# Optimization experiments

Hardware: AMD Instinct MI355X
Metric: run time of the kernel (lower is better)

## Reference

```python
import jax, jax.numpy as jnp
import numpy as np
from jax import lax

B, N = 2, 8192
H = W = 256
KNN_K = 33          # includes self, as in _computeDensity
RADIUS = 0.1
CUTOFF = 1.0        # cutOffThreshold: a dx^2 + b dy^2 + c dx dy <= cutoffC
WIN = 9             # fixed splat footprint (ellipse extents ~1-3 px, clamped at 15 in source)
EPS = 1e-8


def setup_inputs() -> dict:
    key = jax.random.key(0)
    k1, k2, k3, k4, k5 = jax.random.split(key, 5)
    points = jax.random.normal(k1, (B, N, 3), jnp.float32)
    # projected pixel coordinates, kept a few px inside the image
    proj_xy = jax.random.uniform(k2, (B, N, 2), jnp.float32, 4.0, W - 4.0)
    # ellipse coefficients a, b, c with 4ab - c^2 > 0 (valid ellipse)
    ab = jax.random.uniform(k3, (B, N, 2), jnp.float32, 0.1, 0.5)
    c = jax.random.uniform(k4, (B, N, 1), jnp.float32, -0.05, 0.05)
    ellipse_params = jnp.concatenate([ab, c], axis=-1)
    colors = jax.random.uniform(k5, (B, N, 3), jnp.float32)
    return {"points": points, "proj_xy": proj_xy,
            "ellipse_params": ellipse_params, "colors": colors}


def _compute_density(points):
    # faithful jax version of _computeDensity: KNN gaussian density
    r2 = RADIUS * RADIUS
    sq = jnp.sum(points * points, axis=-1)                      # [B,N]
    # pairwise squared distances [B,N,N]
    d2 = sq[:, :, None] + sq[:, None, :] - 2.0 * jnp.einsum('bnd,bmd->bnm', points, points)
    neg_d2k, _ = lax.top_k(-d2, KNN_K)                          # k nearest (incl. self)
    d2k = jnp.maximum(-neg_d2k[:, :, 1:], 0.0)                  # drop self, [B,N,K-1]
    w = jnp.exp(-d2k / r2 / 4.0)
    w = jnp.where(d2k > r2, 0.0, w)
    return jnp.sum(w, axis=-1)                                  # [B,N]


def reference(points, proj_xy, ellipse_params, colors):
    density = _compute_density(points)                          # [B,N]
    a = ellipse_params[..., 0]
    b = ellipse_params[..., 1]
    c = ellipse_params[..., 2]
    x = proj_xy[..., 0]
    y = proj_xy[..., 1]
    # _findEllipseBoundingBox extents, clamped at 15 as in the grad path
    den = 4.0 * a * b - c * c
    xE = jnp.minimum(jnp.sqrt(4.0 * b * CUTOFF / den), 15.0)    # [B,N]
    yE = jnp.minimum(jnp.sqrt(4.0 * a * CUTOFF / den), 15.0)

    # fixed WINxWIN footprint around floor(proj) (jit-friendly bbox)
    R = WIN // 2
    offs = jnp.arange(-R, R + 1, dtype=jnp.float32)
    ox, oy = jnp.meshgrid(offs, offs, indexing='ij')
    ox = ox.reshape(-1)                                         # [P]
    oy = oy.reshape(-1)
    x0 = jnp.floor(x)
    y0 = jnp.floor(y)
    px = x0[..., None] + ox                                     # [B,N,P]
    py = y0[..., None] + oy
    dx = px - x[..., None]
    dy = py - y[..., None]
    # elliptical gaussian splat weight, truncated at cutoff
    Q = a[..., None] * dx * dx + b[..., None] * dy * dy + c[..., None] * dx * dy
    inb = (px >= 0) & (px < W) & (py >= 0) & (py < H)
    bbox = (jnp.abs(dx) <= xE[..., None] + 1.0) & (jnp.abs(dy) <= yE[..., None] + 1.0)
    mask = inb & bbox & (Q <= CUTOFF)
    w = jnp.where(mask, jnp.exp(-0.5 * Q) * density[..., None], 0.0)  # [B,N,P]

    # scatter-accumulate weighted colors and weights per pixel
    pxi = jnp.clip(px.astype(jnp.int32), 0, W - 1)
    pyi = jnp.clip(py.astype(jnp.int32), 0, H - 1)
    bi = jnp.arange(B, dtype=jnp.int32)[:, None, None]
    flat = ((bi * H + pyi) * W + pxi).reshape(-1)               # [B*N*P]
    wc = (w[..., None] * colors[:, :, None, :]).reshape(-1, 3)
    wf = w.reshape(-1)
    img_c = jnp.zeros((B * H * W, 3), jnp.float32).at[flat].add(wc)
    img_w = jnp.zeros((B * H * W,), jnp.float32).at[flat].add(wf)
    image = img_c / (img_w[:, None] + EPS)
    return image.reshape(B, H, W, 3)
```

## Files before the change

### kernel.cpp

```cpp
#include <hip/hip_runtime.h>

#define NB  2
#define NP  8192
#define IMH 256
#define IMW 256
#define NBKT 1024

constexpr float R2F = 0.01f;
constexpr float BK_SCALE = 64.f;
constexpr float BK_OFF   = 8.f;
#define BK_PAD 7

__device__ __forceinline__ int bucket_of(float x) {
    int b = (int)floorf((x + BK_OFF) * BK_SCALE);
    return min(max(b, 0), NBKT - 1);
}

__global__ __launch_bounds__(256) void init_kernel(
    float4* __restrict__ out4, float4* __restrict__ imgw4)
{
    const int t = blockIdx.x * 256 + threadIdx.x;
    const float4 z4 = make_float4(0.f, 0.f, 0.f, 0.f);
    if (t < 98304) out4[t] = z4;
    if (t < 32768) imgw4[t] = z4;
}

__global__ __launch_bounds__(1024) void binsort_kernel(
    const float* __restrict__ pts, float4* __restrict__ sorted,
    int* __restrict__ sidx, int* __restrict__ offsets)
{
    __shared__ int cntA[NBKT], cntB[NBKT], cur[NBKT];
    const int b   = blockIdx.x;
    const int tid = threadIdx.x;
    const float* __restrict__ base = pts + (size_t)b * NP * 3;

    cntA[tid] = 0;
    __syncthreads();

    float xs[8], ys[8], zs[8]; int bks[8];
    #pragma unroll
    for (int k = 0; k < 8; ++k) {
        const int i = k * 1024 + tid;
        xs[k] = base[i * 3 + 0];
        ys[k] = base[i * 3 + 1];
        zs[k] = base[i * 3 + 2];
        bks[k] = bucket_of(xs[k]);
        atomicAdd(&cntA[bks[k]], 1);
    }
    __syncthreads();

    int* src = cntA; int* dst = cntB;
    for (int off = 1; off < NBKT; off <<= 1) {
        int v = src[tid];
        if (tid >= off) v += src[tid - off];
        dst[tid] = v;
        __syncthreads();
        int* tmp = src; src = dst; dst = tmp;
    }
    const int start = (tid == 0) ? 0 : src[tid - 1];
    offsets[b * (NBKT + 1) + tid] = start;
    if (tid == 0) offsets[b * (NBKT + 1) + NBKT] = NP;
    cur[tid] = start;
    __syncthreads();

    #pragma unroll
    for (int k = 0; k < 8; ++k) {
        const int i = k * 1024 + tid;
        const int slot = atomicAdd(&cur[bks[k]], 1);
        const float sq = __fadd_rn(__fadd_rn(__fmul_rn(xs[k], xs[k]),
                                             __fmul_rn(ys[k], ys[k])),
                                   __fmul_rn(zs[k], zs[k]));
        sorted[(size_t)b * NP + slot] = make_float4(xs[k], ys[k], zs[k], sq);
        sidx  [(size_t)b * NP + slot] = i;
    }
}

__global__ __launch_bounds__(256) void densplat_kernel(
    const float4* __restrict__ sorted, const int* __restrict__ sidx,
    const int* __restrict__ offsets,
    const float* __restrict__ proj, const float* __restrict__ ell,
    const float* __restrict__ cols,
    float* __restrict__ img_c, float* __restrict__ img_w)
{
    const int wave = threadIdx.x >> 6, lane = threadIdx.x & 63;
    const int w  = blockIdx.x * 4 + wave;
    const int s0 = w * 8;
    const int b  = s0 >> 13;
    const int sb = s0 & (NP - 1);
    const float4* __restrict__ sp = sorted + (size_t)b * NP;

    float xi[8], yi[8], zi[8], sqi[8], sum[8];
    #pragma unroll
    for (int t = 0; t < 8; ++t) {
        const float4 p = sp[sb + t];
        xi[t] = p.x; yi[t] = p.y; zi[t] = p.z; sqi[t] = p.w;
        sum[t] = 0.f;
    }
    const int blo = max(bucket_of(xi[0]) - BK_PAD, 0);
    const int bhi = min(bucket_of(xi[7]) + BK_PAD + 1, NBKT);
    const int jlo = offsets[b * (NBKT + 1) + blo];
    const int jhi = offsets[b * (NBKT + 1) + bhi];

    for (int jj = jlo + lane; jj < jhi; jj += 64) {
        const float4 pj = sp[jj];
        #pragma unroll
        for (int t = 0; t < 8; ++t) {
            const float dot = __fmaf_rn(zi[t], pj.z,
                              __fmaf_rn(yi[t], pj.y,
                              __fmul_rn(xi[t], pj.x)));
            const float d2 = __fsub_rn(__fadd_rn(sqi[t], pj.w),
                                       __fadd_rn(dot, dot));
            const float d2c = fmaxf(d2, 0.f);
            if (jj != sb + t && d2c <= R2F)
                sum[t] += expf(__fmul_rn(__fdiv_rn(d2c, R2F), -0.25f));
        }
    }

    #pragma unroll
    for (int t = 0; t < 8; ++t) {
        float s = sum[t];
        #pragma unroll
        for (int off2 = 32; off2; off2 >>= 1) s += __shfl_down(s, off2, 64);
        const float dens = __shfl(s, 0, 64);
        if (dens == 0.f) continue;

        const size_t gp = (size_t)b * NP + sidx[(size_t)b * NP + sb + t];
        const float x = proj[gp * 2 + 0], y = proj[gp * 2 + 1];
        const float a  = ell[gp * 3 + 0], bb = ell[gp * 3 + 1], c = ell[gp * 3 + 2];
        const float cr = cols[gp * 3 + 0], cg = cols[gp * 3 + 1], cb = cols[gp * 3 + 2];

        const float den = __fsub_rn(__fmul_rn(__fmul_rn(4.f, a), bb),
                                    __fmul_rn(c, c));
        const float xE = fminf(__fsqrt_rn(__fdiv_rn(__fmul_rn(4.f, bb), den)), 15.f);
        const float yE = fminf(__fsqrt_rn(__fdiv_rn(__fmul_rn(4.f, a),  den)), 15.f);
        const float xEp1 = __fadd_rn(xE, 1.f);
        const float yEp1 = __fadd_rn(yE, 1.f);
        const float x0 = floorf(x), y0 = floorf(y);

        for (int idx = lane; idx < 81; idx += 64) {
            const float ox = (float)(idx / 9) - 4.f;
            const float oy = (float)(idx % 9) - 4.f;
            const float px = __fadd_rn(x0, ox);
            const float py = __fadd_rn(y0, oy);
            if (px < 0.f || px >= 256.f || py < 0.f || py >= 256.f) continue;
            const float dx = __fsub_rn(px, x);
            const float dy = __fsub_rn(py, y);
            if (fabsf(dx) > xEp1 || fabsf(dy) > yEp1) continue;
            const float Q = __fadd_rn(__fadd_rn(__fmul_rn(__fmul_rn(a, dx), dx),
                                                __fmul_rn(__fmul_rn(bb, dy), dy)),
                                      __fmul_rn(__fmul_rn(c, dx), dy));
            if (!(Q <= 1.0f)) continue;
            const float wgt = __fmul_rn(expf(__fmul_rn(-0.5f, Q)), dens);
            const int pxi = (int)px, pyi = (int)py;
            const int flat = ((b << 8) + pyi) * IMW + pxi;
            atomicAdd(&img_c[flat * 3 + 0], __fmul_rn(wgt, cr));
            atomicAdd(&img_c[flat * 3 + 1], __fmul_rn(wgt, cg));
            atomicAdd(&img_c[flat * 3 + 2], __fmul_rn(wgt, cb));
            atomicAdd(&img_w[flat],         wgt);
        }
    }
}

__global__ void norm_kernel(float* __restrict__ out, const float* __restrict__ img_w)
{
    const int p = blockIdx.x * 256 + threadIdx.x;
    if (p < NB * IMH * IMW) {
        const float d = __fadd_rn(img_w[p], 1e-8f);
        out[3 * p + 0] = __fdiv_rn(out[3 * p + 0], d);
        out[3 * p + 1] = __fdiv_rn(out[3 * p + 1], d);
        out[3 * p + 2] = __fdiv_rn(out[3 * p + 2], d);
    }
}

extern "C" void kernel_launch(void* const* d_in, const int* in_sizes, int n_in,
                              void* d_out, int out_size, void* d_ws, size_t ws_size,
                              hipStream_t stream)
{
    const float* points = (const float*)d_in[0];
    const float* proj   = (const float*)d_in[1];
    const float* ell    = (const float*)d_in[2];
    const float* cols   = (const float*)d_in[3];
    float* out = (float*)d_out;

    float4* sorted  = (float4*)d_ws;
    float*  img_w   = (float*)(sorted + (size_t)NB * NP);
    int*    sidx    = (int*)(img_w + (size_t)NB * IMH * IMW);
    int*    offsets = sidx + (size_t)NB * NP;

    init_kernel    <<<384, 256, 0, stream>>>((float4*)out, (float4*)img_w);
    binsort_kernel <<<NB, 1024, 0, stream>>>(points, sorted, sidx, offsets);
    densplat_kernel<<<NB * NP / 32, 256, 0, stream>>>(sorted, sidx, offsets,
                                                      proj, ell, cols, out, img_w);
    norm_kernel    <<<(NB * IMH * IMW + 255) / 256, 256, 0, stream>>>(out, img_w);
}
```

Measured before the change: 41.25 us.

## Fuse init, bin-sort, density-splat and normalize into one persistent kernel with grid barriers

```diff
diff --git a/kernel.cpp b/kernel.cpp
--- a/kernel.cpp
+++ b/kernel.cpp
@@ -5,6 +5,8 @@
 #define IMH 256
 #define IMW 256
 #define NBKT 1024
+#define NBLK 256
+#define NTHR 256
 
 constexpr float R2F = 0.01f;
 constexpr float BK_SCALE = 64.f;
@@ -16,159 +18,190 @@
     return min(max(b, 0), NBKT - 1);
 }
 
-__global__ __launch_bounds__(256) void init_kernel(
-    float4* __restrict__ out4, float4* __restrict__ imgw4)
+__device__ __forceinline__ void gbar(int* __restrict__ bars, int phase) {
+    __syncthreads();
+    if (threadIdx.x == 0) {
+        __threadfence();
+        atomicAdd(&bars[phase], 1);
+        while (__hip_atomic_load(&bars[phase], __ATOMIC_ACQUIRE,
+                                 __HIP_MEMORY_SCOPE_AGENT) < NBLK) {
+            __builtin_amdgcn_s_sleep(2);
+        }
+    }
+    __syncthreads();
+}
+
+__global__ __launch_bounds__(256, 4) void fused_kernel(
+    const float* __restrict__ pts, const float* __restrict__ proj,
+    const float* __restrict__ ell, const float* __restrict__ cols,
+    float* __restrict__ img_c, float* __restrict__ img_w,
+    float4* __restrict__ sorted, int* __restrict__ sidx,
+    int* __restrict__ offsets, int* __restrict__ ghist,
+    int* __restrict__ gcur, int* __restrict__ bars)
 {
-    const int t = blockIdx.x * 256 + threadIdx.x;
-    const float4 z4 = make_float4(0.f, 0.f, 0.f, 0.f);
-    if (t < 98304) out4[t] = z4;
-    if (t < 32768) imgw4[t] = z4;
-}
-
-__global__ __launch_bounds__(1024) void binsort_kernel(
-    const float* __restrict__ pts, float4* __restrict__ sorted,
-    int* __restrict__ sidx, int* __restrict__ offsets)
-{
-    __shared__ int cntA[NBKT], cntB[NBKT], cur[NBKT];
-    const int b   = blockIdx.x;
     const int tid = threadIdx.x;
-    const float* __restrict__ base = pts + (size_t)b * NP * 3;
-
-    cntA[tid] = 0;
-    __syncthreads();
-
-    float xs[8], ys[8], zs[8]; int bks[8];
+    const int t   = blockIdx.x * NTHR + tid;
+
+    {
+        float4* out4  = (float4*)img_c;
+        float4* imgw4 = (float4*)img_w;
+        const float4 z4 = make_float4(0.f, 0.f, 0.f, 0.f);
+        #pragma unroll
+        for (int r = 0; r < 2; ++r) {
+            const int u = t + r * 65536;
+            if (u < 98304) out4[u] = z4;
+            else           imgw4[u - 98304] = z4;
+        }
+        if (t < 512) ((int4*)ghist)[t] = make_int4(0, 0, 0, 0);
+    }
+    gbar(bars, 0);
+
+    if (t < NB * NP) {
+        const float x = pts[(size_t)t * 3];
+        atomicAdd(&ghist[(t >> 13) * NBKT + bucket_of(x)], 1);
+    }
+    gbar(bars, 1);
+
+    if (blockIdx.x == 0) {
+        __shared__ int sA[NTHR], sB[NTHR];
+        for (int b = 0; b < NB; ++b) {
+            const int* gh = ghist + b * NBKT;
+            const int v0 = gh[tid * 4 + 0], v1 = gh[tid * 4 + 1];
+            const int v2 = gh[tid * 4 + 2], v3 = gh[tid * 4 + 3];
+            const int s = v0 + v1 + v2 + v3;
+            sA[tid] = s;
+            __syncthreads();
+            int* src = sA; int* dst = sB;
+            for (int off = 1; off < NTHR; off <<= 1) {
+                int u = src[tid];
+                if (tid >= off) u += src[tid - off];
+                dst[tid] = u;
+                __syncthreads();
+                int* tmp = src; src = dst; dst = tmp;
+            }
+            int start = src[tid] - s;
+            int* ofs = offsets + b * (NBKT + 1);
+            int* gc  = gcur + b * NBKT;
+            ofs[tid * 4 + 0] = start;          gc[tid * 4 + 0] = start;
+            ofs[tid * 4 + 1] = start + v0;     gc[tid * 4 + 1] = start + v0;
+            ofs[tid * 4 + 2] = start + v0 + v1; gc[tid * 4 + 2] = start + v0 + v1;
+            ofs[tid * 4 + 3] = start + v0 + v1 + v2;
+            gc[tid * 4 + 3]  = start + v0 + v1 + v2;
+            if (tid == 0) ofs[NBKT] = NP;
+            __syncthreads();
+        }
+    }
+    gbar(bars, 2);
+
+    if (t < NB * NP) {
+        const int b = t >> 13, i = t & (NP - 1);
+        const float x = pts[(size_t)t * 3 + 0];
+        const float y = pts[(size_t)t * 3 + 1];
+        const float z = pts[(size_t)t * 3 + 2];
+        const int slot = atomicAdd(&gcur[b * NBKT + bucket_of(x)], 1);
+        const float sq = __fadd_rn(__fadd_rn(__fmul_rn(x, x), __fmul_rn(y, y)),
+                                   __fmul_rn(z, z));
+        sorted[(size_t)b * NP + slot] = make_float4(x, y, z, sq);
+        sidx  [(size_t)b * NP + slot] = i;
+    }
+    gbar(bars, 3);
+
+    {
+        const int wave = tid >> 6, lane = tid & 63;
+        const int wid  = blockIdx.x * 4 + wave;
+        for (int g = wid; g < NB * NP / 8; g += 1024) {
+            const int s0 = g * 8;
+            const int b  = s0 >> 13;
+            const int sb = s0 & (NP - 1);
+            const float4* __restrict__ sp = sorted + (size_t)b * NP;
+
+            float xi[8], yi[8], zi[8], sqi[8], sum[8];
+            #pragma unroll
+            for (int u = 0; u < 8; ++u) {
+                const float4 p = sp[sb + u];
+                xi[u] = p.x; yi[u] = p.y; zi[u] = p.z; sqi[u] = p.w;
+                sum[u] = 0.f;
+            }
+            const int blo = max(bucket_of(xi[0]) - BK_PAD, 0);
+            const int bhi = min(bucket_of(xi[7]) + BK_PAD + 1, NBKT);
+            const int jlo = offsets[b * (NBKT + 1) + blo];
+            const int jhi = offsets[b * (NBKT + 1) + bhi];
+
+            for (int jj = jlo + lane; jj < jhi; jj += 64) {
+                const float4 pj = sp[jj];
+                #pragma unroll
+                for (int u = 0; u < 8; ++u) {
+                    const float dot = __fmaf_rn(zi[u], pj.z,
+                                      __fmaf_rn(yi[u], pj.y,
+                                      __fmul_rn(xi[u], pj.x)));
+                    const float d2 = __fsub_rn(__fadd_rn(sqi[u], pj.w),
+                                               __fadd_rn(dot, dot));
+                    const float d2c = fmaxf(d2, 0.f);
+                    if (jj != sb + u && d2c <= R2F)
+                        sum[u] += expf(__fmul_rn(__fdiv_rn(d2c, R2F), -0.25f));
+                }
+            }
+
+            #pragma unroll
+            for (int u = 0; u < 8; ++u) {
+                float s = sum[u];
+                #pragma unroll
+                for (int off2 = 32; off2; off2 >>= 1) s += __shfl_down(s, off2, 64);
+                const float dens = __shfl(s, 0, 64);
+                if (dens == 0.f) continue;
+
+                const size_t gp = (size_t)b * NP + sidx[(size_t)b * NP + sb + u];
+                const float x = proj[gp * 2 + 0], y = proj[gp * 2 + 1];
+                const float a  = ell[gp * 3 + 0], bb = ell[gp * 3 + 1], c = ell[gp * 3 + 2];
+                const float cr = cols[gp * 3 + 0], cg = cols[gp * 3 + 1], cb = cols[gp * 3 + 2];
+
+                const float den = __fsub_rn(__fmul_rn(__fmul_rn(4.f, a), bb),
+                                            __fmul_rn(c, c));
+                const float xE = fminf(__fsqrt_rn(__fdiv_rn(__fmul_rn(4.f, bb), den)), 15.f);
+                const float yE = fminf(__fsqrt_rn(__fdiv_rn(__fmul_rn(4.f, a),  den)), 15.f);
+                const float xEp1 = __fadd_rn(xE, 1.f);
+                const float yEp1 = __fadd_rn(yE, 1.f);
+                const float x0 = floorf(x), y0 = floorf(y);
+
+                for (int idx = lane; idx < 81; idx += 64) {
+                    const float ox = (float)(idx / 9) - 4.f;
+                    const float oy = (float)(idx % 9) - 4.f;
+                    const float px = __fadd_rn(x0, ox);
+                    const float py = __fadd_rn(y0, oy);
+                    if (px < 0.f || px >= 256.f || py < 0.f || py >= 256.f) continue;
+                    const float dx = __fsub_rn(px, x);
+                    const float dy = __fsub_rn(py, y);
+                    if (fabsf(dx) > xEp1 || fabsf(dy) > yEp1) continue;
+                    const float Q = __fadd_rn(__fadd_rn(
+                                        __fmul_rn(__fmul_rn(a, dx), dx),
+                                        __fmul_rn(__fmul_rn(bb, dy), dy)),
+                                      __fmul_rn(__fmul_rn(c, dx), dy));
+                    if (!(Q <= 1.0f)) continue;
+                    const float wgt = __fmul_rn(expf(__fmul_rn(-0.5f, Q)), dens);
+                    const int pxi = (int)px, pyi = (int)py;
+                    const int flat = ((b << 8) + pyi) * IMW + pxi;
+                    atomicAdd(&img_c[flat * 3 + 0], __fmul_rn(wgt, cr));
+                    atomicAdd(&img_c[flat * 3 + 1], __fmul_rn(wgt, cg));
+                    atomicAdd(&img_c[flat * 3 + 2], __fmul_rn(wgt, cb));
+                    atomicAdd(&img_w[flat],         wgt);
+                }
+            }
+        }
+    }
+    gbar(bars, 4);
+
     #pragma unroll
-    for (int k = 0; k < 8; ++k) {
-        const int i = k * 1024 + tid;
-        xs[k] = base[i * 3 + 0];
-        ys[k] = base[i * 3 + 1];
-        zs[k] = base[i * 3 + 2];
-        bks[k] = bucket_of(xs[k]);
-        atomicAdd(&cntA[bks[k]], 1);
-    }
-    __syncthreads();
-
-    int* src = cntA; int* dst = cntB;
-    for (int off = 1; off < NBKT; off <<= 1) {
-        int v = src[tid];
-        if (tid >= off) v += src[tid - off];
-        dst[tid] = v;
-        __syncthreads();
-        int* tmp = src; src = dst; dst = tmp;
-    }
-    const int start = (tid == 0) ? 0 : src[tid - 1];
-    offsets[b * (NBKT + 1) + tid] = start;
-    if (tid == 0) offsets[b * (NBKT + 1) + NBKT] = NP;
-    cur[tid] = start;
-    __syncthreads();
-
-    #pragma unroll
-    for (int k = 0; k < 8; ++k) {
-        const int i = k * 1024 + tid;
-        const int slot = atomicAdd(&cur[bks[k]], 1);
-        const float sq = __fadd_rn(__fadd_rn(__fmul_rn(xs[k], xs[k]),
-                                             __fmul_rn(ys[k], ys[k])),
-                                   __fmul_rn(zs[k], zs[k]));
-        sorted[(size_t)b * NP + slot] = make_float4(xs[k], ys[k], zs[k], sq);
-        sidx  [(size_t)b * NP + slot] = i;
-    }
-}
-
-__global__ __launch_bounds__(256) void densplat_kernel(
-    const float4* __restrict__ sorted, const int* __restrict__ sidx,
-    const int* __restrict__ offsets,
-    const float* __restrict__ proj, const float* __restrict__ ell,
-    const float* __restrict__ cols,
-    float* __restrict__ img_c, float* __restrict__ img_w)
-{
-    const int wave = threadIdx.x >> 6, lane = threadIdx.x & 63;
-    const int w  = blockIdx.x * 4 + wave;
-    const int s0 = w * 8;
-    const int b  = s0 >> 13;
-    const int sb = s0 & (NP - 1);
-    const float4* __restrict__ sp = sorted + (size_t)b * NP;
-
-    float xi[8], yi[8], zi[8], sqi[8], sum[8];
-    #pragma unroll
-    for (int t = 0; t < 8; ++t) {
-        const float4 p = sp[sb + t];
-        xi[t] = p.x; yi[t] = p.y; zi[t] = p.z; sqi[t] = p.w;
-        sum[t] = 0.f;
-    }
-    const int blo = max(bucket_of(xi[0]) - BK_PAD, 0);
-    const int bhi = min(bucket_of(xi[7]) + BK_PAD + 1, NBKT);
-    const int jlo = offsets[b * (NBKT + 1) + blo];
-    const int jhi = offsets[b * (NBKT + 1) + bhi];
-
-    for (int jj = jlo + lane; jj < jhi; jj += 64) {
-        const float4 pj = sp[jj];
+    for (int r = 0; r < 2; ++r) {
+        const int p = t + r * 65536;
+        const float wv = __hip_atomic_load(&img_w[p], __ATOMIC_RELAXED,
+                                           __HIP_MEMORY_SCOPE_AGENT);
+        const float d = __fadd_rn(wv, 1e-8f);
         #pragma unroll
-        for (int t = 0; t < 8; ++t) {
-            const float dot = __fmaf_rn(zi[t], pj.z,
-                              __fmaf_rn(yi[t], pj.y,
-                              __fmul_rn(xi[t], pj.x)));
-            const float d2 = __fsub_rn(__fadd_rn(sqi[t], pj.w),
-                                       __fadd_rn(dot, dot));
-            const float d2c = fmaxf(d2, 0.f);
-            if (jj != sb + t && d2c <= R2F)
-                sum[t] += expf(__fmul_rn(__fdiv_rn(d2c, R2F), -0.25f));
-        }
-    }
-
-    #pragma unroll
-    for (int t = 0; t < 8; ++t) {
-        float s = sum[t];
-        #pragma unroll
-        for (int off2 = 32; off2; off2 >>= 1) s += __shfl_down(s, off2, 64);
-        const float dens = __shfl(s, 0, 64);
-        if (dens == 0.f) continue;
-
-        const size_t gp = (size_t)b * NP + sidx[(size_t)b * NP + sb + t];
-        const float x = proj[gp * 2 + 0], y = proj[gp * 2 + 1];
-        const float a  = ell[gp * 3 + 0], bb = ell[gp * 3 + 1], c = ell[gp * 3 + 2];
-        const float cr = cols[gp * 3 + 0], cg = cols[gp * 3 + 1], cb = cols[gp * 3 + 2];
-
-        const float den = __fsub_rn(__fmul_rn(__fmul_rn(4.f, a), bb),
-                                    __fmul_rn(c, c));
-        const float xE = fminf(__fsqrt_rn(__fdiv_rn(__fmul_rn(4.f, bb), den)), 15.f);
-        const float yE = fminf(__fsqrt_rn(__fdiv_rn(__fmul_rn(4.f, a),  den)), 15.f);
-        const float xEp1 = __fadd_rn(xE, 1.f);
-        const float yEp1 = __fadd_rn(yE, 1.f);
-        const float x0 = floorf(x), y0 = floorf(y);
-
-        for (int idx = lane; idx < 81; idx += 64) {
-            const float ox = (float)(idx / 9) - 4.f;
-            const float oy = (float)(idx % 9) - 4.f;
-            const float px = __fadd_rn(x0, ox);
-            const float py = __fadd_rn(y0, oy);
-            if (px < 0.f || px >= 256.f || py < 0.f || py >= 256.f) continue;
-            const float dx = __fsub_rn(px, x);
-            const float dy = __fsub_rn(py, y);
-            if (fabsf(dx) > xEp1 || fabsf(dy) > yEp1) continue;
-            const float Q = __fadd_rn(__fadd_rn(__fmul_rn(__fmul_rn(a, dx), dx),
-                                                __fmul_rn(__fmul_rn(bb, dy), dy)),
-                                      __fmul_rn(__fmul_rn(c, dx), dy));
-            if (!(Q <= 1.0f)) continue;
-            const float wgt = __fmul_rn(expf(__fmul_rn(-0.5f, Q)), dens);
-            const int pxi = (int)px, pyi = (int)py;
-            const int flat = ((b << 8) + pyi) * IMW + pxi;
-            atomicAdd(&img_c[flat * 3 + 0], __fmul_rn(wgt, cr));
-            atomicAdd(&img_c[flat * 3 + 1], __fmul_rn(wgt, cg));
-            atomicAdd(&img_c[flat * 3 + 2], __fmul_rn(wgt, cb));
-            atomicAdd(&img_w[flat],         wgt);
-        }
-    }
-}
-
-__global__ void norm_kernel(float* __restrict__ out, const float* __restrict__ img_w)
-{
-    const int p = blockIdx.x * 256 + threadIdx.x;
-    if (p < NB * IMH * IMW) {
-        const float d = __fadd_rn(img_w[p], 1e-8f);
-        out[3 * p + 0] = __fdiv_rn(out[3 * p + 0], d);
-        out[3 * p + 1] = __fdiv_rn(out[3 * p + 1], d);
-        out[3 * p + 2] = __fdiv_rn(out[3 * p + 2], d);
+        for (int ch = 0; ch < 3; ++ch) {
+            const float cv = __hip_atomic_load(&img_c[3 * p + ch], __ATOMIC_RELAXED,
+                                               __HIP_MEMORY_SCOPE_AGENT);
+            img_c[3 * p + ch] = __fdiv_rn(cv, d);
+        }
     }
 }
 
@@ -186,10 +219,12 @@
     float*  img_w   = (float*)(sorted + (size_t)NB * NP);
     int*    sidx    = (int*)(img_w + (size_t)NB * IMH * IMW);
     int*    offsets = sidx + (size_t)NB * NP;
-
-    init_kernel    <<<384, 256, 0, stream>>>((float4*)out, (float4*)img_w);
-    binsort_kernel <<<NB, 1024, 0, stream>>>(points, sorted, sidx, offsets);
-    densplat_kernel<<<NB * NP / 32, 256, 0, stream>>>(sorted, sidx, offsets,
-                                                      proj, ell, cols, out, img_w);
-    norm_kernel    <<<(NB * IMH * IMW + 255) / 256, 256, 0, stream>>>(out, img_w);
-}
+    int*    ghist   = offsets + 2052;
+    int*    gcur    = ghist + NB * NBKT;
+    int*    bars    = gcur + NB * NBKT;
+
+    hipMemsetAsync(bars, 0, 64, stream);
+    fused_kernel<<<NBLK, NTHR, 0, stream>>>(points, proj, ell, cols,
+                                            out, img_w, sorted, sidx,
+                                            offsets, ghist, gcur, bars);
+}
```

Result: slower. 132.4 us (+221.0%).

## Replace single-block counting sort with fixed-capacity atomic bins per bucket

Applied to the files above, without the earlier changes.

```diff
diff --git a/kernel.cpp b/kernel.cpp
--- a/kernel.cpp
+++ b/kernel.cpp
@@ -5,6 +5,7 @@
 #define IMH 256
 #define IMW 256
 #define NBKT 1024
+#define CAP 128
 
 constexpr float R2F = 0.01f;
 constexpr float BK_SCALE = 64.f;
@@ -16,115 +17,93 @@
     return min(max(b, 0), NBKT - 1);
 }
 
+__device__ __forceinline__ float sq_np(float x, float y, float z) {
+    return __fadd_rn(__fadd_rn(__fmul_rn(x, x), __fmul_rn(y, y)),
+                     __fmul_rn(z, z));
+}
+
 __global__ __launch_bounds__(256) void init_kernel(
-    float4* __restrict__ out4, float4* __restrict__ imgw4)
+    float4* __restrict__ out4, float4* __restrict__ imgw4, int4* __restrict__ cnt4)
 {
     const int t = blockIdx.x * 256 + threadIdx.x;
     const float4 z4 = make_float4(0.f, 0.f, 0.f, 0.f);
-    if (t < 98304) out4[t] = z4;
-    if (t < 32768) imgw4[t] = z4;
+    if (t < 98304)       out4[t] = z4;
+    else if (t < 131072) imgw4[t - 98304] = z4;
+    if (t < 512)         cnt4[t] = make_int4(0, 0, 0, 0);
 }
 
-__global__ __launch_bounds__(1024) void binsort_kernel(
-    const float* __restrict__ pts, float4* __restrict__ sorted,
-    int* __restrict__ sidx, int* __restrict__ offsets)
+__global__ __launch_bounds__(256) void binfill_kernel(
+    const float* __restrict__ pts, float4* __restrict__ bins,
+    int* __restrict__ counts)
 {
-    __shared__ int cntA[NBKT], cntB[NBKT], cur[NBKT];
-    const int b   = blockIdx.x;
-    const int tid = threadIdx.x;
-    const float* __restrict__ base = pts + (size_t)b * NP * 3;
-
-    cntA[tid] = 0;
-    __syncthreads();
-
-    float xs[8], ys[8], zs[8]; int bks[8];
-    #pragma unroll
-    for (int k = 0; k < 8; ++k) {
-        const int i = k * 1024 + tid;
-        xs[k] = base[i * 3 + 0];
-        ys[k] = base[i * 3 + 1];
-        zs[k] = base[i * 3 + 2];
-        bks[k] = bucket_of(xs[k]);
-        atomicAdd(&cntA[bks[k]], 1);
-    }
-    __syncthreads();
-
-    int* src = cntA; int* dst = cntB;
-    for (int off = 1; off < NBKT; off <<= 1) {
-        int v = src[tid];
-        if (tid >= off) v += src[tid - off];
-        dst[tid] = v;
-        __syncthreads();
-        int* tmp = src; src = dst; dst = tmp;
-    }
-    const int start = (tid == 0) ? 0 : src[tid - 1];
-    offsets[b * (NBKT + 1) + tid] = start;
-    if (tid == 0) offsets[b * (NBKT + 1) + NBKT] = NP;
-    cur[tid] = start;
-    __syncthreads();
-
-    #pragma unroll
-    for (int k = 0; k < 8; ++k) {
-        const int i = k * 1024 + tid;
-        const int slot = atomicAdd(&cur[bks[k]], 1);
-        const float sq = __fadd_rn(__fadd_rn(__fmul_rn(xs[k], xs[k]),
-                                             __fmul_rn(ys[k], ys[k])),
-                                   __fmul_rn(zs[k], zs[k]));
-        sorted[(size_t)b * NP + slot] = make_float4(xs[k], ys[k], zs[k], sq);
-        sidx  [(size_t)b * NP + slot] = i;
-    }
+    const int t = blockIdx.x * 256 + threadIdx.x;
+    const int b = t >> 13, i = t & (NP - 1);
+    const float x = pts[(size_t)t * 3 + 0];
+    const float y = pts[(size_t)t * 3 + 1];
+    const float z = pts[(size_t)t * 3 + 2];
+    const int g = (b << 10) + bucket_of(x);
+    const int slot = atomicAdd(&counts[g], 1);
+    if (slot < CAP)
+        bins[(size_t)g * CAP + slot] = make_float4(x, y, z, __int_as_float(i));
 }
 
-__global__ __launch_bounds__(256) void densplat_kernel(
-    const float4* __restrict__ sorted, const int* __restrict__ sidx,
-    const int* __restrict__ offsets,
+__global__ __launch_bounds__(1024) void densplat_kernel(
+    const float4* __restrict__ bins, const int* __restrict__ counts,
     const float* __restrict__ proj, const float* __restrict__ ell,
     const float* __restrict__ cols,
     float* __restrict__ img_c, float* __restrict__ img_w)
 {
+    const int bk = blockIdx.x;
+    const int b  = bk >> 10, kb = bk & (NBKT - 1);
     const int wave = threadIdx.x >> 6, lane = threadIdx.x & 63;
-    const int w  = blockIdx.x * 4 + wave;
-    const int s0 = w * 8;
-    const int b  = s0 >> 13;
-    const int sb = s0 & (NP - 1);
-    const float4* __restrict__ sp = sorted + (size_t)b * NP;
+    const int cnt = min(counts[bk], CAP);
+    const int s0  = wave * 8;
+    if (s0 >= cnt) return;
+    const int nv = min(8, cnt - s0);
 
     float xi[8], yi[8], zi[8], sqi[8], sum[8];
+    int   oi[8];
     #pragma unroll
-    for (int t = 0; t < 8; ++t) {
-        const float4 p = sp[sb + t];
-        xi[t] = p.x; yi[t] = p.y; zi[t] = p.z; sqi[t] = p.w;
-        sum[t] = 0.f;
+    for (int u = 0; u < 8; ++u) {
+        const int si = s0 + min(u, nv - 1);
+        const float4 p = bins[(size_t)bk * CAP + si];
+        xi[u] = p.x; yi[u] = p.y; zi[u] = p.z;
+        sqi[u] = sq_np(p.x, p.y, p.z);
+        oi[u] = __float_as_int(p.w);
+        sum[u] = 0.f;
     }
-    const int blo = max(bucket_of(xi[0]) - BK_PAD, 0);
-    const int bhi = min(bucket_of(xi[7]) + BK_PAD + 1, NBKT);
-    const int jlo = offsets[b * (NBKT + 1) + blo];
-    const int jhi = offsets[b * (NBKT + 1) + bhi];
 
-    for (int jj = jlo + lane; jj < jhi; jj += 64) {
-        const float4 pj = sp[jj];
-        #pragma unroll
-        for (int t = 0; t < 8; ++t) {
-            const float dot = __fmaf_rn(zi[t], pj.z,
-                              __fmaf_rn(yi[t], pj.y,
-                              __fmul_rn(xi[t], pj.x)));
-            const float d2 = __fsub_rn(__fadd_rn(sqi[t], pj.w),
-                                       __fadd_rn(dot, dot));
-            const float d2c = fmaxf(d2, 0.f);
-            if (jj != sb + t && d2c <= R2F)
-                sum[t] += expf(__fmul_rn(__fdiv_rn(d2c, R2F), -0.25f));
+    const int jb0 = max(kb - BK_PAD, 0), jb1 = min(kb + BK_PAD, NBKT - 1);
+    for (int jb = jb0; jb <= jb1; ++jb) {
+        const int gj = (b << 10) + jb;
+        const int cj = min(counts[gj], CAP);
+        const float4* __restrict__ bp = bins + (size_t)gj * CAP;
+        const bool own = (jb == kb);
+        for (int jj = lane; jj < cj; jj += 64) {
+            const float4 pj = bp[jj];
+            const float sqj = sq_np(pj.x, pj.y, pj.z);
+            #pragma unroll
+            for (int u = 0; u < 8; ++u) {
+                const float dot = __fmaf_rn(zi[u], pj.z,
+                                  __fmaf_rn(yi[u], pj.y,
+                                  __fmul_rn(xi[u], pj.x)));
+                const float d2 = __fsub_rn(__fadd_rn(sqi[u], sqj),
+                                           __fadd_rn(dot, dot));
+                const float d2c = fmaxf(d2, 0.f);
+                if (!(own && jj == s0 + u) && d2c <= R2F)
+                    sum[u] += expf(__fmul_rn(__fdiv_rn(d2c, R2F), -0.25f));
+            }
         }
     }
 
-    #pragma unroll
-    for (int t = 0; t < 8; ++t) {
-        float s = sum[t];
+    for (int u = 0; u < nv; ++u) {
+        float s = sum[u];
         #pragma unroll
         for (int off2 = 32; off2; off2 >>= 1) s += __shfl_down(s, off2, 64);
         const float dens = __shfl(s, 0, 64);
         if (dens == 0.f) continue;
 
-        const size_t gp = (size_t)b * NP + sidx[(size_t)b * NP + sb + t];
+        const size_t gp = (size_t)b * NP + oi[u];
         const float x = proj[gp * 2 + 0], y = proj[gp * 2 + 1];
         const float a  = ell[gp * 3 + 0], bb = ell[gp * 3 + 1], c = ell[gp * 3 + 2];
         const float cr = cols[gp * 3 + 0], cg = cols[gp * 3 + 1], cb = cols[gp * 3 + 2];
@@ -146,9 +125,10 @@
             const float dx = __fsub_rn(px, x);
             const float dy = __fsub_rn(py, y);
             if (fabsf(dx) > xEp1 || fabsf(dy) > yEp1) continue;
-            const float Q = __fadd_rn(__fadd_rn(__fmul_rn(__fmul_rn(a, dx), dx),
-                                                __fmul_rn(__fmul_rn(bb, dy), dy)),
-                                      __fmul_rn(__fmul_rn(c, dx), dy));
+            const float Q = __fadd_rn(__fadd_rn(
+                                __fmul_rn(__fmul_rn(a, dx), dx),
+                                __fmul_rn(__fmul_rn(bb, dy), dy)),
+                              __fmul_rn(__fmul_rn(c, dx), dy));
             if (!(Q <= 1.0f)) continue;
             const float wgt = __fmul_rn(expf(__fmul_rn(-0.5f, Q)), dens);
             const int pxi = (int)px, pyi = (int)py;
@@ -161,7 +141,8 @@
     }
 }
 
-__global__ void norm_kernel(float* __restrict__ out, const float* __restrict__ img_w)
+__global__ __launch_bounds__(256) void norm_kernel(
+    float* __restrict__ out, const float* __restrict__ img_w)
 {
     const int p = blockIdx.x * 256 + threadIdx.x;
     if (p < NB * IMH * IMW) {
@@ -182,14 +163,14 @@
     const float* cols   = (const float*)d_in[3];
     float* out = (float*)d_out;
 
-    float4* sorted  = (float4*)d_ws;
-    float*  img_w   = (float*)(sorted + (size_t)NB * NP);
-    int*    sidx    = (int*)(img_w + (size_t)NB * IMH * IMW);
-    int*    offsets = sidx + (size_t)NB * NP;
+    float4* bins   = (float4*)d_ws;
+    float*  img_w  = (float*)(bins + (size_t)NB * NBKT * CAP);
+    int*    counts = (int*)(img_w + (size_t)NB * IMH * IMW);
 
-    init_kernel    <<<384, 256, 0, stream>>>((float4*)out, (float4*)img_w);
-    binsort_kernel <<<NB, 1024, 0, stream>>>(points, sorted, sidx, offsets);
-    densplat_kernel<<<NB * NP / 32, 256, 0, stream>>>(sorted, sidx, offsets,
-                                                      proj, ell, cols, out, img_w);
+    init_kernel    <<<512, 256, 0, stream>>>((float4*)out, (float4*)img_w,
+                                             (int4*)counts);
+    binfill_kernel <<<NB * NP / 256, 256, 0, stream>>>(points, bins, counts);
+    densplat_kernel<<<NB * NBKT, 1024, 0, stream>>>(bins, counts,
+                                                    proj, ell, cols, out, img_w);
     norm_kernel    <<<(NB * IMH * IMW + 255) / 256, 256, 0, stream>>>(out, img_w);
 }
```

Result: slower. 49.84 us (+20.8%).
